# Performance work log

Hardware: AMD Instinct MI355X
Metric: run time of the kernel (lower is better)

Reference implementation:

```python
import jax, jax.numpy as jnp
import numpy as np

B, HGRID, WGRID = 4, 32, 32
L = 1 + HGRID * WGRID          # cls token + spatial tokens
INPUT_DIM = 512
HEAD_DIM = 512
N_HEAD = 8
QKV_DIM = HEAD_DIM * N_HEAD    # 4096


def pos_embed_2d(h, w, C, dtype):
    """Standard 2D sinusoidal positional embedding, shape (h*w, C)."""
    d = C // 4
    omega = 1.0 / (10000.0 ** (jnp.arange(d, dtype=jnp.float32) / d))
    ey = jnp.arange(h, dtype=jnp.float32)[:, None] * omega      # (h, d)
    ex = jnp.arange(w, dtype=jnp.float32)[:, None] * omega      # (w, d)
    emb_y = jnp.concatenate([jnp.sin(ey), jnp.cos(ey)], -1)     # (h, 2d)
    emb_x = jnp.concatenate([jnp.sin(ex), jnp.cos(ex)], -1)     # (w, 2d)
    emb = jnp.concatenate([
        jnp.broadcast_to(emb_y[:, None, :], (h, w, 2 * d)),
        jnp.broadcast_to(emb_x[None, :, :], (h, w, 2 * d)),
    ], -1)                                                       # (h, w, C)
    return emb.reshape(h * w, C).astype(dtype)


def setup_inputs() -> dict:
    key = jax.random.key(0)
    ks = jax.random.split(key, 16)
    s = 0.02
    inp = {
        "x": jax.random.normal(ks[0], (B, L, INPUT_DIM), dtype=jnp.float32),
        # Q/K/V linear: weight (out, in) as in torch Linear, bias zeros (per _init_bias)
        "Wq": jax.random.normal(ks[1], (QKV_DIM, INPUT_DIM), jnp.float32) * s,
        "bq": jnp.zeros((QKV_DIM,), jnp.float32),
        "Wk": jax.random.normal(ks[2], (QKV_DIM, INPUT_DIM), jnp.float32) * s,
        "bk": jnp.zeros((QKV_DIM,), jnp.float32),
        "Wv": jax.random.normal(ks[3], (QKV_DIM, INPUT_DIM), jnp.float32) * s,
        "bv": jnp.zeros((QKV_DIM,), jnp.float32),
        # 1x1 conv poolers: weight (out_ch, in_ch) = (HEAD_DIM, HEAD_DIM)
        "Wpq": jax.random.normal(ks[4], (HEAD_DIM, HEAD_DIM), jnp.float32) * s,
        "bpq": jax.random.normal(ks[5], (HEAD_DIM,), jnp.float32) * s,
        "Wpk": jax.random.normal(ks[6], (HEAD_DIM, HEAD_DIM), jnp.float32) * s,
        "bpk": jax.random.normal(ks[7], (HEAD_DIM,), jnp.float32) * s,
        "Wpv": jax.random.normal(ks[8], (HEAD_DIM, HEAD_DIM), jnp.float32) * s,
        "bpv": jax.random.normal(ks[9], (HEAD_DIM,), jnp.float32) * s,
        # dispatcher linear: (INPUT_DIM, QKV_DIM)
        "Wd": jax.random.normal(ks[10], (INPUT_DIM, QKV_DIM), jnp.float32) * s,
        "bd": jax.random.normal(ks[11], (INPUT_DIM,), jnp.float32) * s,
        "h": HGRID,
        "w": WGRID,
    }
    return inp


def _pool(t, Wp, bp):
    """AttentionPooler with kernel=1/stride=1: pointwise conv on spatial tokens,
    cls token passed through unchanged. t: (B, n_head, L, head_dim)."""
    cls_tok = t[:, :, :1, :]
    sp = jnp.einsum('bnlc,oc->bnlo', t[:, :, 1:, :], Wp) + bp
    return jnp.concatenate([cls_tok, sp], axis=2)


def reference(x, Wq, bq, Wk, bk, Wv, bv, Wpq, bpq, Wpk, bpk, Wpv, bpv, Wd, bd, h, w):
    Bs, Ls, _ = x.shape

    def proj(Wt, bt):
        y = jnp.einsum('bli,oi->blo', x, Wt) + bt
        return y.reshape(Bs, Ls, N_HEAD, HEAD_DIM).transpose(0, 2, 1, 3)  # (B,nh,L,hd)

    Q = proj(Wq, bq)
    K = proj(Wk, bk)
    V = proj(Wv, bv)

    PQ = _pool(Q, Wpq, bpq)
    PK = _pool(K, Wpk, bpk)
    PV = _pool(V, Wpv, bpv)

    # relative positional encoding added to pooled Q's spatial tokens
    emb = pos_embed_2d(h, w, HEAD_DIM, PQ.dtype)                 # (h*w, hd)
    PQ = jnp.concatenate([PQ[:, :, :1, :], PQ[:, :, 1:, :] + emb], axis=2)

    scale = 1.0 / jnp.sqrt(jnp.asarray(HEAD_DIM, PQ.dtype))
    logits = jnp.einsum('bnqc,bnkc->bnqk', PQ, PK) * scale
    attn = jax.nn.softmax(logits, axis=-1)
    sa = jnp.einsum('bnqk,bnkc->bnqc', attn, PV)

    # skip connection on spatial tokens only (cls row excluded)
    sa = jnp.concatenate([sa[:, :, :1, :], sa[:, :, 1:, :] + Q[:, :, 1:, :]], axis=2)

    stacked = sa.transpose(0, 2, 1, 3).reshape(Bs, Ls, QKV_DIM)
    out = jnp.einsum('blq,oq->blo', stacked, Wd) + bd
    return out
```

## Files before the change

kernel.cpp:

```cpp
#include <hip/hip_runtime.h>


typedef unsigned short u16;
typedef __attribute__((ext_vector_type(8))) short short8;
typedef __attribute__((ext_vector_type(4))) float floatx4;
typedef __attribute__((ext_vector_type(4))) unsigned short us4;

__device__ __forceinline__ u16 f2bf(float f) {
  union { float f; unsigned u; } x; x.f = f;
  unsigned r = (x.u + 0x7fffu + ((x.u >> 16) & 1u)) >> 16;
  return (u16)r;
}
__device__ __forceinline__ float bf2f(u16 u) {
  union { unsigned u; float f; } x; x.u = ((unsigned)u) << 16;
  return x.f;
}

__device__ __forceinline__ void gld_lds16(const void* g, void* l) {
  __builtin_amdgcn_global_load_lds(
      (const __attribute__((address_space(1))) void*)g,
      (__attribute__((address_space(3))) void*)l, 16, 0, 0);
}

struct CvtArgs { const float* src[8]; u16* dst[8]; int n4[8]; };

__global__ __launch_bounds__(256) void cvt_all(CvtArgs a, int total4, float* __restrict__ e) {
  int t = blockIdx.x * 256 + threadIdx.x;
  if (t >= total4) {
    int et = (t - total4) * 4;
    if (et >= 1024 * 512) return;
#pragma unroll
    for (int u = 0; u < 4; ++u) {
      int idx = et + u;
      int c = idx & 511, sp = idx >> 9;
      int y = sp >> 5, xg = sp & 31;
      int j = c & 127, seg = c >> 7;
      float omega = expf(-(float)j * (9.210340371976184f / 128.f));
      float arg = (float)((seg < 2) ? y : xg) * omega;
      e[idx] = (seg & 1) ? cosf(arg) : sinf(arg);
    }
    return;
  }
#pragma unroll
  for (int s = 0; s < 8; ++s) {
    if (t < a.n4[s]) {
      const float* sp = a.src[s] + (long)t * 4;
      u16* dp = a.dst[s] + (long)t * 4;
      float4 v = *(const float4*)sp;
      dp[0] = f2bf(v.x); dp[1] = f2bf(v.y); dp[2] = f2bf(v.z); dp[3] = f2bf(v.w);
      return;
    }
    t -= a.n4[s];
  }
}

__global__ __launch_bounds__(256) void s_edge(const u16* __restrict__ PQ,
                                              const u16* __restrict__ PK,
                                              u16* __restrict__ S, int nh) {
  int flat = blockIdx.x;
  int head, seg;
  if (nh == 32) {
    int xcd = flat & 7, s = flat >> 3;
    head = xcd + 8 * (s >> 3);
    seg = s & 7;
  } else {
    head = flat >> 3;
    seg = flat & 7;
  }
  const u16* pq = PQ + (long)head * 1025 * 512;
  const u16* pk = PK + (long)head * 1025 * 512;
  u16* sh = S + (long)head * 1025 * 1088;
#pragma unroll
  for (int i = 0; i < 2; ++i) {
    int local = i * 256 + (int)threadIdx.x;
    if (local >= 257) continue;
    int e = seg * 257 + local;
    if (e >= 2049) continue;
    int q, kv;
    if (e < 1025) { q = 1024; kv = e; }
    else { q = e - 1025; kv = 1024; }
    const u16* a = pq + (long)q * 512;
    const u16* b = pk + (long)kv * 512;
    float acc = 0.f;
    for (int k8 = 0; k8 < 64; ++k8) {
      short8 av = *(const short8*)(a + k8 * 8);
      short8 bv = *(const short8*)(b + k8 * 8);
#pragma unroll
      for (int u = 0; u < 8; ++u) acc += bf2f((u16)av[u]) * bf2f((u16)bv[u]);
    }
    sh[(long)q * 1088 + kv] = f2bf(acc * 0.04419417382415922f);
  }
}

__global__ __launch_bounds__(256) void softmax_rows(u16* __restrict__ S) {
  int flat = blockIdx.x;
  int xcd = flat & 7, s0 = flat >> 3;
  int zi = s0 / 257, blk = s0 - zi * 257;
  int head = xcd + 8 * zi;
  int wv = threadIdx.x >> 6, lane = threadIdx.x & 63;
  int row_i = blk * 4 + wv;
  if (row_i > 1024) return;
  u16* row = S + ((long)head * 1025 + row_i) * 1088;
  float v[16];
  float mx = -1e30f;
#pragma unroll
  for (int i = 0; i < 4; ++i) {
    us4 p = *(const us4*)(row + i * 256 + lane * 4);
#pragma unroll
    for (int e = 0; e < 4; ++e) { v[i * 4 + e] = bf2f(p[e]); mx = fmaxf(mx, v[i * 4 + e]); }
  }
  float e1024 = (lane == 0) ? bf2f(row[1024]) : -1e30f;
  mx = fmaxf(mx, e1024);
  for (int o = 32; o > 0; o >>= 1) mx = fmaxf(mx, __shfl_xor(mx, o, 64));
  float s = 0.f;
#pragma unroll
  for (int i = 0; i < 16; ++i) { v[i] = __expf(v[i] - mx); s += v[i]; }
  e1024 = (lane == 0) ? __expf(e1024 - mx) : 0.f;
  s += e1024;
  for (int o = 32; o > 0; o >>= 1) s += __shfl_xor(s, o, 64);
  float inv = 1.0f / s;
#pragma unroll
  for (int i = 0; i < 4; ++i) {
    us4 q;
#pragma unroll
    for (int e = 0; e < 4; ++e) q[e] = f2bf(v[i * 4 + e] * inv);
    *(us4*)(row + i * 256 + lane * 4) = q;
  }
  if (lane < 16) {
    us4 q;
#pragma unroll
    for (int e = 0; e < 4; ++e) q[e] = 0;
    if (lane == 0) q[0] = f2bf(e1024 * inv);
    *(us4*)(row + 1024 + lane * 4) = q;
  }
}

__global__ __launch_bounds__(256) void reduce2(const float* __restrict__ part,
                                               const float* __restrict__ bd,
                                               float* __restrict__ out) {
  int t = blockIdx.x * 256 + threadIdx.x;
  long i = (long)t * 4;
  const long STR = 4100ll * 512;
  float4 a = *(const float4*)(part + i);
  float4 b = *(const float4*)(part + i + STR);
  float4 bb = *(const float4*)(bd + (int)(i & 511));
  float4 r;
  r.x = a.x + b.x + bb.x;
  r.y = a.y + b.y + bb.y;
  r.z = a.z + b.z + bb.z;
  r.w = a.w + b.w + bb.w;
  *(float4*)(out + i) = r;
}

struct GP {
  const u16* A; const u16* A2; const u16* B; const u16* B2;
  const float* c0; const float* c1; const float* c2;
  const float* emb; const u16* resid;
  u16* o0; u16* o1; u16* o2;
  u16* p0; u16* p1; u16* p2;
  float* of; int bz0;
};

template <int MODE>
__global__ __launch_bounds__(256) void gemm_bt(GP g) {
  constexpr int KLEN = (MODE == 5) ? 2048 : ((MODE == 4) ? 1088 : 512);
  constexpr int KITER = KLEN / 64;
  constexpr bool LDSEP = (MODE == 0 || MODE == 1 || MODE == 3 || MODE == 4);
  __shared__ u16 smem[16384];
  u16* As = smem;
  u16* Bs = smem + 8192;
  const int tid = threadIdx.x;
  const int lane = tid & 63;
  const int wv = tid >> 6;
  const int wr = wv >> 1, wc = wv & 1;
  const int ccol = lane & 15;
  const int rgrp = lane >> 4;

  int mt, nt, bz;
  if constexpr (MODE == 3 || MODE == 4) {
    constexpr int PER = (MODE == 3) ? 64 : 36;
    constexpr int NTW = (MODE == 3) ? 8 : 4;
    int flat = blockIdx.x;
    int xcd = flat & 7, s = flat >> 3;
    bz = xcd + 8 * (s / PER);
    int tile = s % PER;
    mt = tile / NTW;
    nt = tile % NTW;
  } else if constexpr (MODE == 1) {
    int flat = blockIdx.x;
    int xcd = flat & 7, s = flat >> 3;
    bz = s >> 7;
    int rem = s & 127;
    mt = xcd * 32 + (rem >> 2);
    nt = rem & 3;
  } else if constexpr (MODE == 2) {
    int flat = blockIdx.x;
    int xcd = flat & 7, s = flat >> 3;
    bz = 0;
    mt = xcd * 32 + (s >> 2);
    nt = s & 3;
  } else {
    mt = blockIdx.y; nt = blockIdx.x; bz = blockIdx.z;
  }
  const int gbz = g.bz0 + bz;

  const u16* Ap = g.A;
  const u16* Bp = g.B;
  if constexpr (MODE == 1) {
    if (bz == 1) { Ap = g.A2; Bp = g.B2; }
  }

  int a_row[4], b_row[4], kx[4];
#pragma unroll
  for (int c = 0; c < 4; ++c) {
    int idx = c * 256 + tid;
    int row = idx >> 3;
    kx[c] = ((idx & 7) ^ (row & 7)) * 8;
    {
      int r = mt * 128 + row;
      int off;
      if constexpr (MODE == 0) { r = r < 4099 ? r : 4099; off = r * 512; }
      else if constexpr (MODE == 1 || MODE == 2) { off = ((r >> 10) * 1025 + 1 + (r & 1023)) * 512; }
      else if constexpr (MODE == 3) { off = gbz * (1025 * 512) + r * 512; }
      else if constexpr (MODE == 4) { r = r < 1024 ? r : 1024; off = bz * (1025 * 1088) + r * 1088; }
      else { r = r < 4099 ? r : 4099; off = r * 4096; }
      a_row[c] = off;
    }
    {
      int r = nt * 128 + row;
      int off;
      if constexpr (MODE == 3) { off = gbz * (1025 * 512) + r * 512; }
      else if constexpr (MODE == 4) { off = gbz * (512 * 1088) + r * 1088; }
      else if constexpr (MODE == 5) { off = r * 4096; }
      else { off = r * 512; }
      b_row[c] = off;
    }
  }

  floatx4 acc[4][4];
  {
    float binit[4] = {0.f, 0.f, 0.f, 0.f};
    if constexpr (MODE == 0) {
      int sec = nt >> 5;
      const float* bs = (sec == 0) ? g.c0 : (sec == 1) ? g.c1 : g.c2;
#pragma unroll
      for (int j = 0; j < 4; ++j) binit[j] = bs[(nt & 31) * 128 + wc * 64 + j * 16 + ccol];
    }
    if constexpr (MODE == 1) {
      const float* bs = bz ? g.c1 : g.c0;
#pragma unroll
      for (int j = 0; j < 4; ++j) binit[j] = bs[nt * 128 + wc * 64 + j * 16 + ccol];
    }
    if constexpr (MODE == 2) {
#pragma unroll
      for (int j = 0; j < 4; ++j) binit[j] = g.c0[nt * 128 + wc * 64 + j * 16 + ccol];
    }
#pragma unroll
    for (int i = 0; i < 4; ++i)
#pragma unroll
      for (int j = 0; j < 4; ++j)
#pragma unroll
        for (int rr = 0; rr < 4; ++rr) acc[i][j][rr] = binit[j];
  }

  const int kbase = (MODE == 5) ? bz * 2048 : 0;
  const int l15 = lane & 15;
  const int lq = lane >> 4;
  const int l7 = lane & 7;

  for (int kt = 0; kt < KITER; ++kt) {
    const int k0 = kbase + kt * 64;
#pragma unroll
    for (int c = 0; c < 4; ++c)
      gld_lds16(Ap + a_row[c] + k0 + kx[c], (char*)As + (c * 256 + wv * 64) * 16);
#pragma unroll
    for (int c = 0; c < 4; ++c)
      gld_lds16(Bp + b_row[c] + k0 + kx[c], (char*)Bs + (c * 256 + wv * 64) * 16);
    __syncthreads();
#pragma unroll
    for (int ks = 0; ks < 2; ++ks) {
      const int ch = ((ks * 4 + lq) ^ l7) * 8;
      short8 af[4], bf[4];
#pragma unroll
      for (int i = 0; i < 4; ++i)
        af[i] = *(const short8*)(As + (wr * 64 + i * 16 + l15) * 64 + ch);
#pragma unroll
      for (int j = 0; j < 4; ++j)
        bf[j] = *(const short8*)(Bs + (wc * 64 + j * 16 + l15) * 64 + ch);
#pragma unroll
      for (int i = 0; i < 4; ++i)
#pragma unroll
        for (int j = 0; j < 4; ++j)
          acc[i][j] = __builtin_amdgcn_mfma_f32_16x16x32_bf16(af[i], bf[j], acc[i][j], 0, 0, 0);
    }
    __syncthreads();
  }

  if constexpr (LDSEP) {
#pragma unroll
    for (int i = 0; i < 4; ++i)
#pragma unroll
      for (int j = 0; j < 4; ++j)
#pragma unroll
        for (int rr = 0; rr < 4; ++rr) {
          int lr = wr * 64 + i * 16 + rgrp * 4 + rr;
          int lc = wc * 64 + j * 16 + ccol;
          float v = acc[i][j][rr];
          if constexpr (MODE == 3) v *= 0.04419417382415922f;
          smem[lr * 128 + (lc ^ (rgrp << 4))] = f2bf(v);
        }
    __syncthreads();
#pragma unroll
    for (int q = 0; q < 8; ++q) {
      int cid = q * 256 + tid;
      int r = cid >> 4;
      int c = cid & 15;
      int pc = c ^ ((((unsigned)r >> 2) & 3) << 1);
      short8 val = *(const short8*)(smem + r * 128 + pc * 8);
      int grow = mt * 128 + r;
      if constexpr (MODE == 0) {
        if (grow < 4100) {
          int sec = nt >> 5;
          int col = (nt & 31) * 128 + c * 8;
          u16* ob = (sec == 0) ? g.o0 : (sec == 1) ? g.o1 : g.o2;
          int b = grow / 1025, l = grow - b * 1025;
          int n = col >> 9, ch2 = col & 511;
          long bn = (long)b * 8 + n;
          *(short8*)(ob + (bn * 1025 + l) * 512 + ch2) = val;
          if (l == 0) {
            if (sec == 0) *(short8*)(g.p0 + (bn * 1025 + 1024) * 512 + ch2) = val;
            else if (sec == 1) *(short8*)(g.p1 + (bn * 1025 + 1024) * 512 + ch2) = val;
            else {
#pragma unroll
              for (int e = 0; e < 8; ++e)
                g.p2[(bn * 512 + ch2 + e) * 1088 + 1024] = (u16)val[e];
            }
          }
        }
      } else if constexpr (MODE == 1) {
        int bn = grow >> 10, sp = grow & 1023;
        int gcol = nt * 128 + c * 8;
        short8 outv = val;
        if (bz == 0) {
          const float* ep = g.emb + sp * 512 + gcol;
          float4 e0 = *(const float4*)ep;
          float4 e1 = *(const float4*)(ep + 4);
          float ee[8] = {e0.x, e0.y, e0.z, e0.w, e1.x, e1.y, e1.z, e1.w};
#pragma unroll
          for (int e = 0; e < 8; ++e) outv[e] = (short)f2bf(bf2f((u16)val[e]) + ee[e]);
        }
        u16* dst = (bz == 0) ? g.o0 : g.o1;
        *(short8*)(dst + ((long)bn * 1025 + sp) * 512 + gcol) = outv;
      } else if constexpr (MODE == 3) {
        *(short8*)(g.o0 + ((long)bz * 1025 + grow) * 1088 + nt * 128 + c * 8) = val;
      } else {
        if (grow <= 1024) {
          int gcol0 = nt * 128 + c * 8;
          short8 outv = val;
          int l = (grow == 1024) ? 0 : grow + 1;
          if (grow < 1024) {
            short8 rs = *(const short8*)(g.resid + ((long)gbz * 1025 + l) * 512 + gcol0);
#pragma unroll
            for (int e = 0; e < 8; ++e)
              outv[e] = (short)f2bf(bf2f((u16)val[e]) + bf2f((u16)rs[e]));
          }
          int b = gbz >> 3, n = gbz & 7;
          *(short8*)(g.o0 + (((long)b * 1025 + l) * 8 + n) * 512 + gcol0) = outv;
        }
      }
    }
  } else if constexpr (MODE == 2) {
#pragma unroll
    for (int i = 0; i < 4; ++i)
#pragma unroll
      for (int j = 0; j < 4; ++j)
#pragma unroll
        for (int rr = 0; rr < 4; ++rr) {
          int lr2 = wc * 64 + j * 16 + ccol;
          int lc2 = wr * 64 + i * 16 + rgrp * 4 + rr;
          smem[lr2 * 128 + (lc2 ^ ((lr2 & 15) << 3))] = f2bf(acc[i][j][rr]);
        }
    __syncthreads();
    {
      int bn = mt >> 3, sp0 = (mt & 7) * 128;
#pragma unroll
      for (int q = 0; q < 8; ++q) {
        int cid = q * 256 + tid;
        int r = cid >> 4;
        int c = cid & 15;
        int pc = c ^ (r & 15);
        short8 val = *(const short8*)(smem + r * 128 + pc * 8);
        int ch = nt * 128 + r;
        *(short8*)(g.o0 + ((long)(bn * 512 + ch)) * 1088 + sp0 + c * 8) = val;
      }
    }
  } else {
#pragma unroll
    for (int i = 0; i < 4; ++i) {
#pragma unroll
      for (int j = 0; j < 4; ++j) {
        const int gcol = nt * 128 + wc * 64 + j * 16 + ccol;
#pragma unroll
        for (int rr = 0; rr < 4; ++rr) {
          const int grow = mt * 128 + wr * 64 + i * 16 + rgrp * 4 + rr;
          if (grow < 4100)
            g.of[((long)bz * 4100 + grow) * 512 + gcol] = acc[i][j][rr];
        }
      }
    }
  }
}

extern "C" void kernel_launch(void* const* d_in, const int* in_sizes, int n_in,
                              void* d_out, int out_size, void* d_ws, size_t ws_size,
                              hipStream_t stream) {
  const float* x   = (const float*)d_in[0];
  const float* Wq  = (const float*)d_in[1];
  const float* bq  = (const float*)d_in[2];
  const float* Wk  = (const float*)d_in[3];
  const float* bk  = (const float*)d_in[4];
  const float* Wv  = (const float*)d_in[5];
  const float* bv  = (const float*)d_in[6];
  const float* Wpq = (const float*)d_in[7];
  const float* bpq = (const float*)d_in[8];
  const float* Wpk = (const float*)d_in[9];
  const float* bpk = (const float*)d_in[10];
  const float* Wpv = (const float*)d_in[11];
  const float* bpv = (const float*)d_in[12];
  const float* Wd  = (const float*)d_in[13];
  const float* bd  = (const float*)d_in[14];
  float* out = (float*)d_out;

  char* ws = (char*)d_ws;
  size_t off = 0;
  auto alloc = [&](size_t bytes) {
    char* p = ws + off;
    off += (bytes + 255) & ~(size_t)255;
    return p;
  };
  u16* Wpqb = (u16*)alloc(512ull * 512 * 2);
  u16* Wpkb = (u16*)alloc(512ull * 512 * 2);
  u16* Wpvb = (u16*)alloc(512ull * 512 * 2);
  u16* Wdb  = (u16*)alloc(4096ull * 512 * 2);
  u16* Q    = (u16*)alloc(32ull * 1025 * 512 * 2);
  u16* PQ   = (u16*)alloc(32ull * 1025 * 512 * 2);
  u16* PK   = (u16*)alloc(32ull * 1025 * 512 * 2);
  u16* PVt  = (u16*)alloc(32ull * 512 * 1088 * 2);
  size_t s_off = off;
  u16* K    = (u16*)alloc(32ull * 1025 * 512 * 2);
  u16* V    = (u16*)alloc(32ull * 1025 * 512 * 2);
  u16* xb   = (u16*)alloc(4100ull * 512 * 2);
  u16* Wqb  = (u16*)alloc(4096ull * 512 * 2);
  u16* Wkb  = (u16*)alloc(4096ull * 512 * 2);
  u16* Wvb  = (u16*)alloc(4096ull * 512 * 2);
  float* embp = (float*)alloc(1024ull * 512 * 4);
  size_t fixed_need = off;
  u16* S = (u16*)(ws + s_off);
  float* part = (float*)PQ;
  (void)in_sizes; (void)n_in; (void)out_size;

  const size_t sbytes = 1025ull * 1088 * 2;
  size_t need1 = s_off + 32ull * sbytes;
  size_t need2 = s_off + 16ull * sbytes;
  size_t stk4_off = s_off + ((8ull * sbytes + 255) & ~(size_t)255);
  size_t need4 = stk4_off + 4100ull * 4096 * 2;
  int nchunk;
  u16* stk;
  if (ws_size >= need1)      { nchunk = 1; stk = PK; }
  else if (ws_size >= need2 && ws_size >= fixed_need) { nchunk = 2; stk = PK; }
  else if (ws_size >= need4 && ws_size >= fixed_need) {
    nchunk = 4; stk = (u16*)(ws + stk4_off);
  } else return;
  if (nchunk == 2) {
    size_t stk2_off = s_off + ((16ull * sbytes + 255) & ~(size_t)255);
    if (ws_size >= stk2_off + 4100ull * 4096 * 2) stk = (u16*)(ws + stk2_off);
    else {
      nchunk = 4;
      if (ws_size >= need4) stk = (u16*)(ws + stk4_off);
      else return;
    }
  }
  int hpc = 32 / nchunk;

  CvtArgs ca;
  ca.src[0] = x;   ca.dst[0] = xb;   ca.n4[0] = 4100 * 512 / 4;
  ca.src[1] = Wq;  ca.dst[1] = Wqb;  ca.n4[1] = 4096 * 512 / 4;
  ca.src[2] = Wk;  ca.dst[2] = Wkb;  ca.n4[2] = 4096 * 512 / 4;
  ca.src[3] = Wv;  ca.dst[3] = Wvb;  ca.n4[3] = 4096 * 512 / 4;
  ca.src[4] = Wpq; ca.dst[4] = Wpqb; ca.n4[4] = 512 * 512 / 4;
  ca.src[5] = Wpk; ca.dst[5] = Wpkb; ca.n4[5] = 512 * 512 / 4;
  ca.src[6] = Wpv; ca.dst[6] = Wpvb; ca.n4[6] = 512 * 512 / 4;
  ca.src[7] = Wd;  ca.dst[7] = Wdb;  ca.n4[7] = 512 * 4096 / 4;
  int total4 = 0;
  for (int s = 0; s < 8; ++s) total4 += ca.n4[s];
  int grid1 = (total4 + 1024 * 512 / 4 + 255) / 256;
  cvt_all<<<grid1, 256, 0, stream>>>(ca, total4, embp);

  {
    GP g = {};
    g.A = xb; g.B = Wqb;
    g.c0 = bq; g.c1 = bk; g.c2 = bv;
    g.o0 = Q; g.o1 = K; g.o2 = V;
    g.p0 = PQ; g.p1 = PK; g.p2 = PVt;
    gemm_bt<0><<<dim3(96, 33, 1), 256, 0, stream>>>(g);
  }

  {
    GP g = {};
    g.A = Q; g.A2 = K; g.B = Wpqb; g.B2 = Wpkb;
    g.c0 = bpq; g.c1 = bpk; g.emb = embp;
    g.o0 = PQ; g.o1 = PK;
    gemm_bt<1><<<dim3(2048, 1, 1), 256, 0, stream>>>(g);
  }
  {
    GP g = {};
    g.A = V; g.B = Wpvb; g.c0 = bpv; g.o0 = PVt;
    gemm_bt<2><<<dim3(1024, 1, 1), 256, 0, stream>>>(g);
  }

  for (int c = 0; c < nchunk; ++c) {
    GP g3 = {}; g3.A = PQ; g3.B = PK; g3.o0 = S; g3.bz0 = c * hpc;
    gemm_bt<3><<<dim3(64 * hpc, 1, 1), 256, 0, stream>>>(g3);
    s_edge<<<hpc * 8, 256, 0, stream>>>(
        PQ + (long)c * hpc * 1025 * 512, PK + (long)c * hpc * 1025 * 512, S, hpc);
    softmax_rows<<<257 * hpc, 256, 0, stream>>>(S);
    GP g4 = {}; g4.A = S; g4.B = PVt; g4.resid = Q; g4.o0 = stk; g4.bz0 = c * hpc;
    gemm_bt<4><<<dim3(36 * hpc, 1, 1), 256, 0, stream>>>(g4);
  }

  {
    GP g = {}; g.A = stk; g.B = Wdb; g.of = part;
    gemm_bt<5><<<dim3(4, 33, 2), 256, 0, stream>>>(g);
  }
  reduce2<<<(4100 * 512 / 4 + 255) / 256, 256, 0, stream>>>(part, bd, out);
}
```

Before: 443.4 us.

## Fold pooler weights into QKV projections and compute pooled outputs directly

Precomputes combined weights Wp·W per head with a new GEMM mode and folded biases, so the spatial-token pooled PQ, PK and PVt come straight from x in one GEMM. The separate Q/K/V-then-pool GEMM chain and the K and V intermediate buffers are dropped. Q is still produced for the residual, and the cls-token rows are handled by a small scalar kernel. This removes one large intermediate round trip through memory, but adds a weight-combining GEMM on every call and changes the bf16 rounding order.

```diff
diff --git a/kernel.cpp b/kernel.cpp
--- a/kernel.cpp
+++ b/kernel.cpp
@@ -51,6 +51,63 @@
       return;
     }
     t -= a.n4[s];
+  }
+}
+
+struct CF {
+  const u16* W;
+  const u16* Wp;
+  const u16* xb;
+  const float *bq, *bk, *bv, *bpq, *bpk, *bpv;
+  u16 *PQ, *PK, *PVt;
+  float* bc;
+};
+
+__global__ __launch_bounds__(256) void cls_fold(CF a) {
+  int t = blockIdx.x * 256 + threadIdx.x;
+  if (t < 12288) {
+    int mat = t >> 12, o2 = t & 4095, n = o2 >> 9, ch = o2 & 511;
+    const float* bsrc = (mat == 0) ? a.bq : (mat == 1) ? a.bk : a.bv;
+    float ac[4];
+    float bias = bsrc[o2];
+#pragma unroll
+    for (int b = 0; b < 4; ++b) ac[b] = bias;
+    const u16* w = a.W + (long)t * 512;
+    for (int k8 = 0; k8 < 64; ++k8) {
+      short8 wv = *(const short8*)(w + k8 * 8);
+      float wf[8];
+#pragma unroll
+      for (int e = 0; e < 8; ++e) wf[e] = bf2f((u16)wv[e]);
+#pragma unroll
+      for (int b = 0; b < 4; ++b) {
+        short8 xv = *(const short8*)(a.xb + ((long)b * 1025) * 512 + k8 * 8);
+#pragma unroll
+        for (int e = 0; e < 8; ++e) ac[b] += wf[e] * bf2f((u16)xv[e]);
+      }
+    }
+#pragma unroll
+    for (int b = 0; b < 4; ++b) {
+      long bn = b * 8 + n;
+      u16 v = f2bf(ac[b]);
+      if (mat == 0)      a.PQ[(bn * 1025 + 1024) * 512 + ch] = v;
+      else if (mat == 1) a.PK[(bn * 1025 + 1024) * 512 + ch] = v;
+      else               a.PVt[(bn * 512 + ch) * 1088 + 1024] = v;
+    }
+  } else {
+    int t2 = t - 12288;
+    if (t2 >= 12288) return;
+    int mat = t2 >> 12, o2 = t2 & 4095, n = o2 >> 9, o = o2 & 511;
+    const u16* wp = a.Wp + mat * 262144 + o * 512;
+    const float* bsrc = (mat == 0) ? a.bq : (mat == 1) ? a.bk : a.bv;
+    const float* bpp = (mat == 0) ? a.bpq : (mat == 1) ? a.bpk : a.bpv;
+    float s = bpp[o];
+    for (int k8 = 0; k8 < 64; ++k8) {
+      short8 wv = *(const short8*)(wp + k8 * 8);
+      const float* bb = bsrc + n * 512 + k8 * 8;
+#pragma unroll
+      for (int e = 0; e < 8; ++e) s += bf2f((u16)wv[e]) * bb[e];
+    }
+    a.bc[t2] = s;
   }
 }
 
@@ -165,7 +222,6 @@
 __global__ __launch_bounds__(256) void gemm_bt(GP g) {
   constexpr int KLEN = (MODE == 5) ? 2048 : ((MODE == 4) ? 1088 : 512);
   constexpr int KITER = KLEN / 64;
-  constexpr bool LDSEP = (MODE == 0 || MODE == 1 || MODE == 3 || MODE == 4);
   __shared__ u16 smem[16384];
   u16* As = smem;
   u16* Bs = smem + 8192;
@@ -176,7 +232,7 @@
   const int ccol = lane & 15;
   const int rgrp = lane >> 4;
 
-  int mt, nt, bz;
+  int mt, nt, bz, mh = 0;
   if constexpr (MODE == 3 || MODE == 4) {
     constexpr int PER = (MODE == 3) ? 64 : 36;
     constexpr int NTW = (MODE == 3) ? 8 : 4;
@@ -186,19 +242,11 @@
     int tile = s % PER;
     mt = tile / NTW;
     nt = tile % NTW;
-  } else if constexpr (MODE == 1) {
+  } else if constexpr (MODE == 6) {
     int flat = blockIdx.x;
-    int xcd = flat & 7, s = flat >> 3;
-    bz = s >> 7;
-    int rem = s & 127;
-    mt = xcd * 32 + (rem >> 2);
-    nt = rem & 3;
-  } else if constexpr (MODE == 2) {
-    int flat = blockIdx.x;
-    int xcd = flat & 7, s = flat >> 3;
-    bz = 0;
-    mt = xcd * 32 + (s >> 2);
-    nt = s & 3;
+    mh = flat >> 4;
+    int tile = flat & 15;
+    mt = tile >> 2; nt = tile & 3; bz = 0;
   } else {
     mt = blockIdx.y; nt = blockIdx.x; bz = blockIdx.z;
   }
@@ -206,8 +254,8 @@
 
   const u16* Ap = g.A;
   const u16* Bp = g.B;
-  if constexpr (MODE == 1) {
-    if (bz == 1) { Ap = g.A2; Bp = g.B2; }
+  if constexpr (MODE == 0) {
+    if (nt >= 96) Bp = g.B2;
   }
 
   int a_row[4], b_row[4], kx[4];
@@ -219,20 +267,26 @@
     {
       int r = mt * 128 + row;
       int off;
-      if constexpr (MODE == 0) { r = r < 4099 ? r : 4099; off = r * 512; }
-      else if constexpr (MODE == 1 || MODE == 2) { off = ((r >> 10) * 1025 + 1 + (r & 1023)) * 512; }
+      if constexpr (MODE == 0) { off = ((r >> 10) * 1025 + 1 + (r & 1023)) * 512; }
       else if constexpr (MODE == 3) { off = gbz * (1025 * 512) + r * 512; }
       else if constexpr (MODE == 4) { r = r < 1024 ? r : 1024; off = bz * (1025 * 1088) + r * 1088; }
+      else if constexpr (MODE == 6) { off = (mh >> 3) * 262144 + r * 512; }
       else { r = r < 4099 ? r : 4099; off = r * 4096; }
       a_row[c] = off;
     }
     {
-      int r = nt * 128 + row;
       int off;
-      if constexpr (MODE == 3) { off = gbz * (1025 * 512) + r * 512; }
-      else if constexpr (MODE == 4) { off = gbz * (512 * 1088) + r * 1088; }
-      else if constexpr (MODE == 5) { off = r * 4096; }
-      else { off = r * 512; }
+      if constexpr (MODE == 6) {
+        int rb = idx >> 4, s2 = idx & 15;
+        int cg = (s2 - ((rb >> 3) << 1)) & 15;
+        off = mh * 262144 + rb * 512 + nt * 128 + cg * 8;
+      } else {
+        int r = nt * 128 + row;
+        if constexpr (MODE == 0) { off = ((nt >= 96) ? (r - 12288) : r) * 512; }
+        else if constexpr (MODE == 3) { off = gbz * (1025 * 512) + r * 512; }
+        else if constexpr (MODE == 4) { off = gbz * (512 * 1088) + r * 1088; }
+        else { off = r * 4096; }
+      }
       b_row[c] = off;
     }
   }
@@ -242,18 +296,9 @@
     float binit[4] = {0.f, 0.f, 0.f, 0.f};
     if constexpr (MODE == 0) {
       int sec = nt >> 5;
-      const float* bs = (sec == 0) ? g.c0 : (sec == 1) ? g.c1 : g.c2;
+      const float* bs = (sec < 3) ? (g.c0 + sec * 4096) : g.c1;
 #pragma unroll
       for (int j = 0; j < 4; ++j) binit[j] = bs[(nt & 31) * 128 + wc * 64 + j * 16 + ccol];
-    }
-    if constexpr (MODE == 1) {
-      const float* bs = bz ? g.c1 : g.c0;
-#pragma unroll
-      for (int j = 0; j < 4; ++j) binit[j] = bs[nt * 128 + wc * 64 + j * 16 + ccol];
-    }
-    if constexpr (MODE == 2) {
-#pragma unroll
-      for (int j = 0; j < 4; ++j) binit[j] = g.c0[nt * 128 + wc * 64 + j * 16 + ccol];
     }
 #pragma unroll
     for (int i = 0; i < 4; ++i)
@@ -274,29 +319,113 @@
     for (int c = 0; c < 4; ++c)
       gld_lds16(Ap + a_row[c] + k0 + kx[c], (char*)As + (c * 256 + wv * 64) * 16);
 #pragma unroll
-    for (int c = 0; c < 4; ++c)
-      gld_lds16(Bp + b_row[c] + k0 + kx[c], (char*)Bs + (c * 256 + wv * 64) * 16);
+    for (int c = 0; c < 4; ++c) {
+      if constexpr (MODE == 6)
+        gld_lds16(Bp + b_row[c] + k0 * 512, (char*)Bs + (c * 256 + wv * 64) * 16);
+      else
+        gld_lds16(Bp + b_row[c] + k0 + kx[c], (char*)Bs + (c * 256 + wv * 64) * 16);
+    }
     __syncthreads();
 #pragma unroll
     for (int ks = 0; ks < 2; ++ks) {
       const int ch = ((ks * 4 + lq) ^ l7) * 8;
-      short8 af[4], bf[4];
+      short8 af[4], bfr[4];
 #pragma unroll
       for (int i = 0; i < 4; ++i)
         af[i] = *(const short8*)(As + (wr * 64 + i * 16 + l15) * 64 + ch);
-#pragma unroll
-      for (int j = 0; j < 4; ++j)
-        bf[j] = *(const short8*)(Bs + (wc * 64 + j * 16 + l15) * 64 + ch);
+      if constexpr (MODE == 6) {
+#pragma unroll
+        for (int j = 0; j < 4; ++j) {
+          int ro = ((wc * 64 + j * 16 + l15) + ((ks * 4 + lq) << 4)) & 127;
+          const u16* bp2 = Bs + (ks * 32 + lq * 8) * 128 + ro;
+          short8 tv;
+#pragma unroll
+          for (int e = 0; e < 8; ++e) tv[e] = (short)bp2[e * 128];
+          bfr[j] = tv;
+        }
+      } else {
+#pragma unroll
+        for (int j = 0; j < 4; ++j)
+          bfr[j] = *(const short8*)(Bs + (wc * 64 + j * 16 + l15) * 64 + ch);
+      }
 #pragma unroll
       for (int i = 0; i < 4; ++i)
 #pragma unroll
         for (int j = 0; j < 4; ++j)
-          acc[i][j] = __builtin_amdgcn_mfma_f32_16x16x32_bf16(af[i], bf[j], acc[i][j], 0, 0, 0);
+          acc[i][j] = __builtin_amdgcn_mfma_f32_16x16x32_bf16(af[i], bfr[j], acc[i][j], 0, 0, 0);
     }
     __syncthreads();
   }
 
-  if constexpr (LDSEP) {
+  if constexpr (MODE == 0) {
+    const int sec = nt >> 5;
+    if (sec == 2) {
+#pragma unroll
+      for (int i = 0; i < 4; ++i)
+#pragma unroll
+        for (int j = 0; j < 4; ++j)
+#pragma unroll
+          for (int rr = 0; rr < 4; ++rr) {
+            int lr2 = wc * 64 + j * 16 + ccol;
+            int lc2 = wr * 64 + i * 16 + rgrp * 4 + rr;
+            smem[lr2 * 128 + (lc2 ^ ((lr2 & 15) << 3))] = f2bf(acc[i][j][rr]);
+          }
+      __syncthreads();
+      {
+        int b = mt >> 3, sp0 = (mt & 7) * 128;
+        int nt2 = nt & 31, n = nt2 >> 2, ch0 = (nt2 & 3) * 128;
+        long bn = b * 8 + n;
+#pragma unroll
+        for (int q = 0; q < 8; ++q) {
+          int cid = q * 256 + tid;
+          int r = cid >> 4;
+          int c = cid & 15;
+          int pc = c ^ (r & 15);
+          short8 val = *(const short8*)(smem + r * 128 + pc * 8);
+          *(short8*)(g.p2 + (bn * 512 + ch0 + r) * 1088 + sp0 + c * 8) = val;
+        }
+      }
+    } else {
+#pragma unroll
+      for (int i = 0; i < 4; ++i)
+#pragma unroll
+        for (int j = 0; j < 4; ++j)
+#pragma unroll
+          for (int rr = 0; rr < 4; ++rr) {
+            int lr = wr * 64 + i * 16 + rgrp * 4 + rr;
+            int lc = wc * 64 + j * 16 + ccol;
+            smem[lr * 128 + (lc ^ (rgrp << 4))] = f2bf(acc[i][j][rr]);
+          }
+      __syncthreads();
+#pragma unroll
+      for (int q = 0; q < 8; ++q) {
+        int cid = q * 256 + tid;
+        int r = cid >> 4;
+        int c = cid & 15;
+        int pc = c ^ ((((unsigned)r >> 2) & 3) << 1);
+        short8 val = *(const short8*)(smem + r * 128 + pc * 8);
+        int grow = mt * 128 + r;
+        int b = grow >> 10, sp = grow & 1023;
+        int gcol = (nt & 31) * 128 + c * 8;
+        int n = gcol >> 9, ch2 = gcol & 511;
+        long bn = b * 8 + n;
+        if (sec == 0) {
+          const float* ep = g.emb + sp * 512 + ch2;
+          float4 e0 = *(const float4*)ep;
+          float4 e1 = *(const float4*)(ep + 4);
+          float ee[8] = {e0.x, e0.y, e0.z, e0.w, e1.x, e1.y, e1.z, e1.w};
+          short8 outv;
+#pragma unroll
+          for (int e = 0; e < 8; ++e) outv[e] = (short)f2bf(bf2f((u16)val[e]) + ee[e]);
+          *(short8*)(g.o0 + (bn * 1025 + sp) * 512 + ch2) = outv;
+        } else if (sec == 1) {
+          *(short8*)(g.o1 + (bn * 1025 + sp) * 512 + ch2) = val;
+        } else {
+          *(short8*)(g.o2 + (bn * 1025 + 1 + sp) * 512 + ch2) = val;
+        }
+      }
+    }
+  } else if constexpr (MODE == 3 || MODE == 4 || MODE == 6) {
 #pragma unroll
     for (int i = 0; i < 4; ++i)
 #pragma unroll
@@ -318,41 +447,10 @@
       int pc = c ^ ((((unsigned)r >> 2) & 3) << 1);
       short8 val = *(const short8*)(smem + r * 128 + pc * 8);
       int grow = mt * 128 + r;
-      if constexpr (MODE == 0) {
-        if (grow < 4100) {
-          int sec = nt >> 5;
-          int col = (nt & 31) * 128 + c * 8;
-          u16* ob = (sec == 0) ? g.o0 : (sec == 1) ? g.o1 : g.o2;
-          int b = grow / 1025, l = grow - b * 1025;
-          int n = col >> 9, ch2 = col & 511;
-          long bn = (long)b * 8 + n;
-          *(short8*)(ob + (bn * 1025 + l) * 512 + ch2) = val;
-          if (l == 0) {
-            if (sec == 0) *(short8*)(g.p0 + (bn * 1025 + 1024) * 512 + ch2) = val;
-            else if (sec == 1) *(short8*)(g.p1 + (bn * 1025 + 1024) * 512 + ch2) = val;
-            else {
-#pragma unroll
-              for (int e = 0; e < 8; ++e)
-                g.p2[(bn * 512 + ch2 + e) * 1088 + 1024] = (u16)val[e];
-            }
-          }
-        }
-      } else if constexpr (MODE == 1) {
-        int bn = grow >> 10, sp = grow & 1023;
-        int gcol = nt * 128 + c * 8;
-        short8 outv = val;
-        if (bz == 0) {
-          const float* ep = g.emb + sp * 512 + gcol;
-          float4 e0 = *(const float4*)ep;
-          float4 e1 = *(const float4*)(ep + 4);
-          float ee[8] = {e0.x, e0.y, e0.z, e0.w, e1.x, e1.y, e1.z, e1.w};
-#pragma unroll
-          for (int e = 0; e < 8; ++e) outv[e] = (short)f2bf(bf2f((u16)val[e]) + ee[e]);
-        }
-        u16* dst = (bz == 0) ? g.o0 : g.o1;
-        *(short8*)(dst + ((long)bn * 1025 + sp) * 512 + gcol) = outv;
-      } else if constexpr (MODE == 3) {
+      if constexpr (MODE == 3) {
         *(short8*)(g.o0 + ((long)bz * 1025 + grow) * 1088 + nt * 128 + c * 8) = val;
+      } else if constexpr (MODE == 6) {
+        *(short8*)(g.o0 + ((long)(mh * 512) + grow) * 512 + nt * 128 + c * 8) = val;
       } else {
         if (grow <= 1024) {
           int gcol0 = nt * 128 + c * 8;
@@ -367,31 +465,6 @@
           int b = gbz >> 3, n = gbz & 7;
           *(short8*)(g.o0 + (((long)b * 1025 + l) * 8 + n) * 512 + gcol0) = outv;
         }
-      }
-    }
-  } else if constexpr (MODE == 2) {
-#pragma unroll
-    for (int i = 0; i < 4; ++i)
-#pragma unroll
-      for (int j = 0; j < 4; ++j)
-#pragma unroll
-        for (int rr = 0; rr < 4; ++rr) {
-          int lr2 = wc * 64 + j * 16 + ccol;
-          int lc2 = wr * 64 + i * 16 + rgrp * 4 + rr;
-          smem[lr2 * 128 + (lc2 ^ ((lr2 & 15) << 3))] = f2bf(acc[i][j][rr]);
-        }
-    __syncthreads();
-    {
-      int bn = mt >> 3, sp0 = (mt & 7) * 128;
-#pragma unroll
-      for (int q = 0; q < 8; ++q) {
-        int cid = q * 256 + tid;
-        int r = cid >> 4;
-        int c = cid & 15;
-        int pc = c ^ (r & 15);
-        short8 val = *(const short8*)(smem + r * 128 + pc * 8);
-        int ch = nt * 128 + r;
-        *(short8*)(g.o0 + ((long)(bn * 512 + ch)) * 1088 + sp0 + c * 8) = val;
       }
     }
   } else {
@@ -447,17 +520,18 @@
   u16* PK   = (u16*)alloc(32ull * 1025 * 512 * 2);
   u16* PVt  = (u16*)alloc(32ull * 512 * 1088 * 2);
   size_t s_off = off;
-  u16* K    = (u16*)alloc(32ull * 1025 * 512 * 2);
-  u16* V    = (u16*)alloc(32ull * 1025 * 512 * 2);
   u16* xb   = (u16*)alloc(4100ull * 512 * 2);
   u16* Wqb  = (u16*)alloc(4096ull * 512 * 2);
   u16* Wkb  = (u16*)alloc(4096ull * 512 * 2);
   u16* Wvb  = (u16*)alloc(4096ull * 512 * 2);
+  u16* Wc   = (u16*)alloc(3ull * 4096 * 512 * 2);
+  float* bc = (float*)alloc(3ull * 4096 * 4);
   float* embp = (float*)alloc(1024ull * 512 * 4);
   size_t fixed_need = off;
   u16* S = (u16*)(ws + s_off);
   float* part = (float*)PQ;
-  (void)in_sizes; (void)n_in; (void)out_size;
+  (void)in_sizes; (void)n_in; (void)out_size; (void)Wkb; (void)Wvb;
+  (void)Wpkb; (void)Wpvb;
 
   const size_t sbytes = 1025ull * 1088 * 2;
   size_t need1 = s_off + 32ull * sbytes;
@@ -498,24 +572,24 @@
 
   {
     GP g = {};
-    g.A = xb; g.B = Wqb;
-    g.c0 = bq; g.c1 = bk; g.c2 = bv;
-    g.o0 = Q; g.o1 = K; g.o2 = V;
-    g.p0 = PQ; g.p1 = PK; g.p2 = PVt;
-    gemm_bt<0><<<dim3(96, 33, 1), 256, 0, stream>>>(g);
+    g.A = Wpqb; g.B = Wqb; g.o0 = Wc;
+    gemm_bt<6><<<dim3(384, 1, 1), 256, 0, stream>>>(g);
+  }
+  {
+    CF cf;
+    cf.W = Wqb; cf.Wp = Wpqb; cf.xb = xb;
+    cf.bq = bq; cf.bk = bk; cf.bv = bv;
+    cf.bpq = bpq; cf.bpk = bpk; cf.bpv = bpv;
+    cf.PQ = PQ; cf.PK = PK; cf.PVt = PVt; cf.bc = bc;
+    cls_fold<<<96, 256, 0, stream>>>(cf);
   }
 
   {
     GP g = {};
-    g.A = Q; g.A2 = K; g.B = Wpqb; g.B2 = Wpkb;
-    g.c0 = bpq; g.c1 = bpk; g.emb = embp;
-    g.o0 = PQ; g.o1 = PK;
-    gemm_bt<1><<<dim3(2048, 1, 1), 256, 0, stream>>>(g);
-  }
-  {
-    GP g = {};
-    g.A = V; g.B = Wpvb; g.c0 = bpv; g.o0 = PVt;
-    gemm_bt<2><<<dim3(1024, 1, 1), 256, 0, stream>>>(g);
+    g.A = xb; g.B = Wc; g.B2 = Wqb;
+    g.c0 = bc; g.c1 = bq; g.emb = embp;
+    g.o0 = PQ; g.o1 = PK; g.o2 = Q; g.p2 = PVt;
+    gemm_bt<0><<<dim3(128, 32, 1), 256, 0, stream>>>(g);
   }
 
   for (int c = 0; c < nchunk; ++c) {
```

After: 464.2 us. 4.7% more time.
